# Performance work log

Hardware: AMD Instinct MI355X
Metric: run time of the kernel (lower is better)

Reference implementation:

```python
import jax, jax.numpy as jnp
import numpy as np

RRELU_SLOPE = (1.0 / 8.0 + 1.0 / 3.0) / 2.0  # F.rrelu eval mode
N_ENT, N_REL2, H, E, B, T = 20000, 460, 128, 400000, 1024, 8


def _lin(x, W, b):
    return x @ W.T + b  # torch nn.Linear convention


def _gru_cell(x, h, w_ih, w_hh, b_ih, b_hh):
    gi = x @ w_ih.T + b_ih
    gh = h @ w_hh.T + b_hh
    i_r, i_z, i_n = jnp.split(gi, 3, axis=1)
    h_r, h_z, h_n = jnp.split(gh, 3, axis=1)
    r = jax.nn.sigmoid(i_r + h_r)
    z = jax.nn.sigmoid(i_z + h_z)
    n = jnp.tanh(i_n + r * h_n)
    return (1.0 - z) * n + z * h


def setup_inputs() -> dict:
    key = jax.random.key(0)
    ks = jax.random.split(key, 24)
    s = 0.02
    inp = {
        'ent_emb': jax.random.normal(ks[0], (N_ENT, H), jnp.float32),
        'rel_emb': jax.random.normal(ks[1], (N_REL2, H), jnp.float32),
        'weight_neighbor': jax.random.normal(ks[2], (H, H), jnp.float32) * s,
        'loop_weight': jax.random.normal(ks[3], (H, H), jnp.float32) * s,
        'evolve_loop_weight': jax.random.normal(ks[4], (H, H), jnp.float32) * s,
        'w_ih': jax.random.normal(ks[5], (3 * H, H), jnp.float32) * s,
        'w_hh': jax.random.normal(ks[6], (3 * H, H), jnp.float32) * s,
        'b_ih': jnp.zeros((3 * H,), jnp.float32),
        'b_hh': jnp.zeros((3 * H,), jnp.float32),
        'W_map1': jax.random.normal(ks[7], (2 * H, H), jnp.float32) * s,
        'b_map1': jnp.zeros((2 * H,), jnp.float32),
        'W_map2': jax.random.normal(ks[8], (H, 2 * H), jnp.float32) * s,
        'b_map2': jnp.zeros((H,), jnp.float32),
        'W_h1': jax.random.normal(ks[9], (H, H), jnp.float32) * s,
        'b_h1': jnp.zeros((H,), jnp.float32),
        'W_h2': jax.random.normal(ks[10], (H, H), jnp.float32) * s,
        'b_h2': jnp.zeros((H,), jnp.float32),
        'W_align': jax.random.normal(ks[11], (H, H), jnp.float32) * s,
        'b_align': jnp.zeros((H,), jnp.float32),
        'W_attn': jax.random.normal(ks[12], (H, H), jnp.float32) * s,
        'b_attn': jnp.zeros((H,), jnp.float32),
    }
    u = jax.random.uniform(ks[13], (B, T * N_REL2), jnp.float32)
    mask = jax.random.uniform(ks[14], (B, T * N_REL2)) > 0.7  # sparse history
    inp['partial_embeding'] = u * mask
    inp['edge_src'] = jax.random.randint(ks[15], (E,), 0, N_ENT, jnp.int32)
    inp['edge_dst'] = jax.random.randint(ks[16], (E,), 0, N_ENT, jnp.int32)
    inp['edge_type'] = jax.random.randint(ks[17], (E,), 0, N_REL2, jnp.int32)
    sub = jax.random.randint(ks[18], (B,), 0, N_ENT, jnp.int32)
    rel = jax.random.randint(ks[19], (B,), 0, N_REL2, jnp.int32)
    obj = jax.random.randint(ks[20], (B,), 0, N_ENT, jnp.int32)
    inp['triples'] = jnp.stack([sub, rel, obj], axis=1)
    return inp


def reference(ent_emb, rel_emb, weight_neighbor, loop_weight, evolve_loop_weight,
              w_ih, w_hh, b_ih, b_hh, W_map1, b_map1, W_map2, b_map2,
              W_h1, b_h1, W_h2, b_h2, W_align, b_align, W_attn, b_attn,
              partial_embeding, edge_src, edge_dst, edge_type, triples):
    # ---- UnionRGCNLayer: gather-transform-scatter ----
    h = ent_emb
    msg = (h[edge_src] + rel_emb[edge_type]) @ weight_neighbor          # [E, H]
    agg = jax.ops.segment_sum(msg, edge_dst, num_segments=N_ENT)        # [N, H]
    deg = jax.ops.segment_sum(jnp.ones((edge_dst.shape[0],), h.dtype), edge_dst,
                              num_segments=N_ENT)
    norm = jnp.where(deg > 0, 1.0 / jnp.where(deg > 0, deg, 1.0), 0.0)[:, None]
    loop = jnp.where((deg > 0)[:, None], h @ loop_weight, h @ evolve_loop_weight)
    x = agg * norm + loop
    pre_emb = jnp.where(x >= 0, x, x * RRELU_SLOPE)                     # rrelu (eval)

    # ---- PathPredictor.forward_back ----
    mapped_rel = _lin(_lin(rel_emb, W_map1, b_map1), W_map2, b_map2)    # [2R, H]
    q_rel = mapped_rel[triples[:, 1]]                                   # [B, H]
    A = _lin(q_rel, W_attn, b_attn) @ mapped_rel.T                      # [B, 2R]
    hist = partial_embeding.reshape(B, T, N_REL2).transpose(1, 0, 2)    # [T, B, 2R]

    def step(gh, cur):
        attn = cur * A
        attn = jax.nn.softmax(jnp.where(attn == 0, -1e9, attn), axis=1)
        rel_path = attn @ mapped_rel                                    # [B, H]
        return _gru_cell(rel_path, gh, w_ih, w_hh, b_ih, b_hh), None

    gru_hidden, _ = jax.lax.scan(step, jnp.zeros((B, H), pre_emb.dtype), hist)
    predicted_hist = 0.1 * _lin(_lin(q_rel, W_h1, b_h1), W_h2, b_h2) + q_rel
    match_loss = jnp.mean((predicted_hist - gru_hidden) ** 2)

    # ---- forward_forth, distmult scoring ----
    gh2 = _gru_cell(q_rel, predicted_hist, w_ih, w_hh, b_ih, b_hh)      # [B, H]
    sub_emb = pre_emb[triples[:, 0]]
    aligned_all = _lin(pre_emb, W_align, b_align)                       # [N, H]
    score_ = (_lin(sub_emb, W_align, b_align) * gh2) @ aligned_all.T    # [B, N]
    score = jax.nn.sigmoid(score_)
    # BCE(score, one_hot(obj)) without materializing labels:
    logp = jax.nn.log_sigmoid(score_)
    log1mp = jax.nn.log_sigmoid(-score_)
    total = -jnp.sum(log1mp)
    rows = jnp.arange(B)
    total = total + jnp.sum(log1mp[rows, triples[:, 2]] - logp[rows, triples[:, 2]])
    path_loss = total / (B * N_ENT)
    return score, match_loss, path_loss
```

## Files before the change

kernel.cpp:

```cpp
#include <hip/hip_runtime.h>

typedef unsigned short u16;
typedef unsigned int u32;
typedef __attribute__((ext_vector_type(8))) short bf8v;
typedef __attribute__((ext_vector_type(4))) float f4v;

#define RRELU_SLOPE 0.22916666667f

__device__ inline float bf2f(u16 u){ unsigned int i = ((unsigned int)u) << 16; float f; __builtin_memcpy(&f, &i, 4); return f; }
__device__ inline u16 f2bf(float f){ unsigned int i; __builtin_memcpy(&i, &f, 4); unsigned int r = (i + 0x7fffu + ((i >> 16) & 1u)) >> 16; return (u16)r; }
__device__ inline float fsigm(float x){ return 1.f / (1.f + __expf(-x)); }
__device__ inline float ftanh(float x){ return 2.f / (1.f + __expf(-2.f * x)) - 1.f; }

__global__ __launch_bounds__(256) void prep_k(
    const float* __restrict__ Wn, const float* __restrict__ Wl, const float* __restrict__ We,
    const float* __restrict__ wih, const float* __restrict__ whh,
    const float* __restrict__ m1, const float* __restrict__ m2,
    const float* __restrict__ h1, const float* __restrict__ h2,
    const float* __restrict__ attn, const float* __restrict__ alg, const float* __restrict__ rel,
    u16* __restrict__ Bcat, u16* __restrict__ wihb, u16* __restrict__ whhb,
    u16* __restrict__ m1b, u16* __restrict__ m2b, u16* __restrict__ h1b, u16* __restrict__ h2b,
    u16* __restrict__ attnb, u16* __restrict__ algb, u16* __restrict__ relb)
{
    int id = blockIdx.x * 256 + threadIdx.x;
    if (id < 49152) {
        int n = id / 384, k = id % 384;
        float v = (k < 128) ? Wn[k*128 + n] : (k < 256 ? Wl[(k-128)*128 + n] : We[(k-256)*128 + n]);
        Bcat[id] = f2bf(v); return;
    }
    id -= 49152;
    if (id < 49152) { wihb[id] = f2bf(wih[id]); return; } id -= 49152;
    if (id < 49152) { whhb[id] = f2bf(whh[id]); return; } id -= 49152;
    if (id < 32768) { m1b[id]  = f2bf(m1[id]);  return; } id -= 32768;
    if (id < 32768) { m2b[id]  = f2bf(m2[id]);  return; } id -= 32768;
    if (id < 16384) { h1b[id]  = f2bf(h1[id]);  return; } id -= 16384;
    if (id < 16384) { h2b[id]  = f2bf(h2[id]);  return; } id -= 16384;
    if (id < 16384) { attnb[id]= f2bf(attn[id]);return; } id -= 16384;
    if (id < 16384) { algb[id] = f2bf(alg[id]); return; } id -= 16384;
    if (id < 58880) { relb[id] = f2bf(rel[id]); return; }
}

__global__ __launch_bounds__(256) void entcast_k(
    const float* __restrict__ ent, u16* __restrict__ entb)
{
    int id = blockIdx.x * 256 + threadIdx.x;
    entb[id] = f2bf(ent[id]);
}

__global__ __launch_bounds__(256) void hist_k(
    const int* __restrict__ dst, int* __restrict__ hist, int E)
{
    int e = blockIdx.x * 256 + threadIdx.x;
    if (e < E) atomicAdd(&hist[dst[e]], 1);
}

__global__ __launch_bounds__(1024) void scan_k(
    const int* __restrict__ hist, int* __restrict__ starts, int* __restrict__ cursor)
{
    __shared__ int part[1024];
    int t = threadIdx.x;
    int base = t * 20;
    int s = 0;
    for (int j = 0; j < 20; ++j) { int idx = base + j; if (idx < 20000) s += hist[idx]; }
    part[t] = s;
    __syncthreads();
    for (int off = 1; off < 1024; off <<= 1) {
        int v = (t >= off) ? part[t - off] : 0;
        __syncthreads();
        part[t] += v;
        __syncthreads();
    }
    int run = (t > 0) ? part[t - 1] : 0;
    for (int j = 0; j < 20; ++j) {
        int idx = base + j;
        if (idx < 20000) { starts[idx] = run; cursor[idx] = run; run += hist[idx]; }
    }
    if (t == 1023) starts[20000] = run;
}

__global__ __launch_bounds__(256) void scatter_k(
    const int* __restrict__ src, const int* __restrict__ dst, const int* __restrict__ typ,
    int* __restrict__ cursor, int2* __restrict__ spack, int E)
{
    int e = blockIdx.x * 256 + threadIdx.x;
    if (e >= E) return;
    int d = dst[e];
    int p = atomicAdd(&cursor[d], 1);
    spack[p] = make_int2(src[e], typ[e]);
}

__global__ __launch_bounds__(64) void agg_acat_k(
    const int2* __restrict__ spack, const int* __restrict__ starts,
    const u32* __restrict__ hb, const u32* __restrict__ rb, u32* __restrict__ Acat32)
{
    int i = blockIdx.x;
    int lane = threadIdx.x;
    int s0 = starts[i], s1 = starts[i + 1];
    float sx = 0.f, sy = 0.f;
    for (int e = s0; e < s1; ++e) {
        int2 st = spack[e];
        u32 a = hb[(long)st.x * 64 + lane];
        u32 r = rb[(long)st.y * 64 + lane];
        sx += bf2f((u16)(a & 0xffff)) + bf2f((u16)(r & 0xffff));
        sy += bf2f((u16)(a >> 16))    + bf2f((u16)(r >> 16));
    }
    bool has = s1 > s0;
    float nrm = has ? 1.f / (float)(s1 - s0) : 0.f;
    u32 hv = hb[(long)i * 64 + lane];
    u32 agg = (u32)f2bf(sx * nrm) | ((u32)f2bf(sy * nrm) << 16);
    long o = (long)i * 192 + lane;
    Acat32[o]       = agg;
    Acat32[o + 64]  = has ? hv : 0u;
    Acat32[o + 128] = has ? 0u : hv;
}

__global__ __launch_bounds__(256) void gemm_nt(
    const u16* __restrict__ A, const u16* __restrict__ B, const float* __restrict__ bias,
    float* __restrict__ Cf, u16* __restrict__ Cbf, u16* __restrict__ CT,
    const u16* __restrict__ residb, const int* __restrict__ arows,
    int M, int N, int K, int lda, int ldb, int ldc, int ldct, int arow_stride,
    float rscale, int epi)
{
    int tid = threadIdx.x;
    int wave = tid >> 6, lane = tid & 63;
    int ln = lane & 15, q = lane >> 4;
    int bm = blockIdx.y * 64 + wave * 16;
    int bn = blockIdx.x * 64;
    int am = bm + ln; if (am >= M) am = M - 1;
    long ar = arows ? (long)arows[(long)am * arow_stride] : (long)am;
    const u16* Ap = A + ar * lda;
    int br[4];
#pragma unroll
    for (int nt = 0; nt < 4; ++nt) { int n = bn + nt*16 + ln; br[nt] = (n < N) ? n : (N - 1); }
    f4v acc[4] = {};
    for (int kc = 0; kc < K; kc += 32) {
        bf8v af = *(const bf8v*)(Ap + kc + q*8);
#pragma unroll
        for (int nt = 0; nt < 4; ++nt) {
            bf8v bv = *(const bf8v*)(B + (long)br[nt]*ldb + kc + q*8);
            acc[nt] = __builtin_amdgcn_mfma_f32_16x16x32_bf16(af, bv, acc[nt], 0, 0, 0);
        }
    }
#pragma unroll
    for (int nt = 0; nt < 4; ++nt) {
        int n = bn + nt*16 + ln;
        if (n >= N) continue;
        float bv = bias ? bias[n] : 0.f;
#pragma unroll
        for (int r = 0; r < 4; ++r) {
            int m = bm + q*4 + r;
            if (m >= M) continue;
            float v = acc[nt][r] + bv;
            if (epi == 1) v = (v >= 0.f) ? v : v * RRELU_SLOPE;
            if (residb)  v = rscale * v + bf2f(residb[(long)m*ldc + n]);
            long ci = (long)m*ldc + n;
            if (Cf)  Cf[ci]  = v;
            if (Cbf) Cbf[ci] = f2bf(v);
            if (CT)  CT[(long)n*ldct + m] = f2bf(v);
        }
    }
}

__global__ __launch_bounds__(256) void qrel_k(
    const u16* __restrict__ mapb, const int* __restrict__ trip,
    u16* __restrict__ qrelb, u16* __restrict__ X)
{
    int id = blockIdx.x * 256 + threadIdx.x;
    int b = id >> 7, k = id & 127;
    int r = trip[b*3 + 1];
    u16 v = mapb[r*128 + k];
    qrelb[id] = v;
    X[(long)(8192 + b)*128 + k] = v;
}

__global__ __launch_bounds__(64) void softmax_k(
    const float* __restrict__ Amat, const float* __restrict__ part, u16* __restrict__ Xattn)
{
    int row = blockIdx.x;
    int t = row >> 10, b = row & 1023;
    int lane = threadIdx.x;
    const float* arow = Amat + (long)b*460;
    const float* crow = part + (long)b*3680 + t*460;
    float v[8], e[8];
    float m = -1e30f;
#pragma unroll
    for (int i = 0; i < 8; ++i) {
        int r = i*64 + lane;
        e[i] = 0.f;
        if (r < 460) {
            float x = crow[r] * arow[r];
            x = (x == 0.f) ? -1e9f : x;
            v[i] = x; m = fmaxf(m, x);
        } else v[i] = -1e30f;
    }
#pragma unroll
    for (int off = 32; off; off >>= 1) m = fmaxf(m, __shfl_xor(m, off));
    float sum = 0.f;
#pragma unroll
    for (int i = 0; i < 8; ++i) {
        int r = i*64 + lane;
        if (r < 460) { e[i] = __expf(v[i] - m); sum += e[i]; }
    }
#pragma unroll
    for (int off = 32; off; off >>= 1) sum += __shfl_xor(sum, off);
    float inv = 1.f / sum;
#pragma unroll
    for (int i = 0; i < 8; ++i) {
        int r = i*64 + lane;
        if (r < 460)      Xattn[(long)row*480 + r] = f2bf(e[i] * inv);
        else if (r < 480) Xattn[(long)row*480 + r] = 0;
    }
}

__global__ __launch_bounds__(256) void gru_k(
    const float* __restrict__ gi, const u16* __restrict__ whhb, const float* __restrict__ bhh,
    const float* __restrict__ pred, float* __restrict__ gh2, float* __restrict__ match_acc)
{
    __shared__ u16  hbf[16][136];
    __shared__ float hf [4][128];
    __shared__ float ghl[4][388];
    __shared__ float red[4];
    int tid = threadIdx.x;
    int wave = tid >> 6, lane = tid & 63;
    int ln = lane & 15, q = lane >> 4;
    int bb = blockIdx.x * 4;
    for (int i = tid; i < 16*136; i += 256) hbf[i/136][i%136] = 0;
    for (int i = tid; i < 4*128; i += 256) hf[i>>7][i&127] = 0.f;
    bf8v bfrag[6][4];
#pragma unroll
    for (int nt = 0; nt < 6; ++nt)
#pragma unroll
        for (int kc = 0; kc < 4; ++kc)
            bfrag[nt][kc] = *(const bf8v*)(whhb + (long)(wave*96 + nt*16 + ln)*128 + kc*32 + q*8);
    int k = tid & 127;
    float br = bhh[k], bz = bhh[128 + k], bn_ = bhh[256 + k];
    __syncthreads();
    float msum = 0.f;
    for (int t = 0; t <= 8; ++t) {
        float gr[2], gz[2], gn[2], pv[2];
        long girow0 = (t < 8) ? ((long)t*1024 + bb) : (8192 + bb);
#pragma unroll
        for (int it = 0; it < 2; ++it) {
            int m = it*2 + (tid >> 7);
            const float* gp = gi + (girow0 + m)*384;
            gr[it] = gp[k]; gz[it] = gp[128 + k]; gn[it] = gp[256 + k];
            pv[it] = (t >= 7) ? pred[(long)(bb + m)*128 + k] : 0.f;
        }
        if (t == 8) {
#pragma unroll
            for (int it = 0; it < 2; ++it) {
                int m = it*2 + (tid >> 7);
                hf[m][k] = pv[it]; hbf[m][k] = f2bf(pv[it]);
            }
            __syncthreads();
        }
        f4v acc[6] = {};
#pragma unroll
        for (int kc = 0; kc < 4; ++kc) {
            bf8v af = *(const bf8v*)&hbf[ln][kc*32 + q*8];
#pragma unroll
            for (int nt = 0; nt < 6; ++nt)
                acc[nt] = __builtin_amdgcn_mfma_f32_16x16x32_bf16(af, bfrag[nt][kc], acc[nt], 0, 0, 0);
        }
        if (q == 0) {
#pragma unroll
            for (int nt = 0; nt < 6; ++nt)
#pragma unroll
                for (int r = 0; r < 4; ++r)
                    ghl[r][wave*96 + nt*16 + ln] = acc[nt][r];
        }
        __syncthreads();
#pragma unroll
        for (int it = 0; it < 2; ++it) {
            int m = it*2 + (tid >> 7);
            float rr = fsigm(gr[it] + ghl[m][k] + br);
            float zz = fsigm(gz[it] + ghl[m][128 + k] + bz);
            float nn = ftanh(gn[it] + rr * (ghl[m][256 + k] + bn_));
            float hn = (1.f - zz) * nn + zz * hf[m][k];
            if (t == 7) { float d = pv[it] - hn; msum += d*d; }
            if (t == 8) { gh2[(long)(bb + m)*128 + k] = hn; }
            else        { hf[m][k] = hn; hbf[m][k] = f2bf(hn); }
        }
        __syncthreads();
    }
#pragma unroll
    for (int off = 32; off; off >>= 1) msum += __shfl_down(msum, off);
    if (lane == 0) red[wave] = msum;
    __syncthreads();
    if (tid == 0) atomicAdd(match_acc, red[0] + red[1] + red[2] + red[3]);
}

__global__ __launch_bounds__(256) void vmul_k(
    const float* __restrict__ subl, const float* __restrict__ gh2, u16* __restrict__ V)
{
    int id = blockIdx.x * 256 + threadIdx.x;
    V[id] = f2bf(subl[id] * gh2[id]);
}

__global__ __launch_bounds__(256) void score_k(
    const u16* __restrict__ V, const u16* __restrict__ AL,
    float* __restrict__ out, float* __restrict__ sp_acc, int N)
{
    int tid = threadIdx.x;
    int wave = tid >> 6, lane = tid & 63;
    int ln = lane & 15, q = lane >> 4;
    int bm = blockIdx.y * 128 + (wave >> 1) * 64;
    int bn = blockIdx.x * 128 + (wave & 1) * 64;
    int br[4];
#pragma unroll
    for (int nt = 0; nt < 4; ++nt) { int n = bn + nt*16 + ln; br[nt] = (n < N) ? n : (N - 1); }
    f4v acc[4][4] = {};
    for (int kc = 0; kc < 128; kc += 32) {
        bf8v a[4], b[4];
#pragma unroll
        for (int mt = 0; mt < 4; ++mt)
            a[mt] = *(const bf8v*)(V + (long)(bm + mt*16 + ln)*128 + kc + q*8);
#pragma unroll
        for (int nt = 0; nt < 4; ++nt)
            b[nt] = *(const bf8v*)(AL + (long)br[nt]*128 + kc + q*8);
#pragma unroll
        for (int mt = 0; mt < 4; ++mt)
#pragma unroll
            for (int nt = 0; nt < 4; ++nt)
                acc[mt][nt] = __builtin_amdgcn_mfma_f32_16x16x32_bf16(a[mt], b[nt], acc[mt][nt], 0, 0, 0);
    }
    float lsum = 0.f;
#pragma unroll
    for (int mt = 0; mt < 4; ++mt)
#pragma unroll
    for (int nt = 0; nt < 4; ++nt) {
        int n = bn + nt*16 + ln;
        if (n >= N) continue;
#pragma unroll
        for (int r = 0; r < 4; ++r) {
            int m = bm + mt*16 + q*4 + r;
            float s = acc[mt][nt][r];
            float e = __expf(-fabsf(s));
            float inv = 1.f / (1.f + e);
            __builtin_nontemporal_store((s >= 0.f) ? inv : e * inv, &out[(long)m*N + n]);
            lsum += fmaxf(s, 0.f) + __logf(1.f + e);
        }
    }
#pragma unroll
    for (int off = 32; off; off >>= 1) lsum += __shfl_xor(lsum, off);
    __shared__ float red[4];
    if (lane == 0) red[wave] = lsum;
    __syncthreads();
    if (tid == 0) atomicAdd(sp_acc, red[0] + red[1] + red[2] + red[3]);
}

__global__ __launch_bounds__(64) void objdot_k(
    const u16* __restrict__ V, const u16* __restrict__ AL, const int* __restrict__ trip,
    float* __restrict__ obj_acc)
{
    int b = blockIdx.x, lane = threadIdx.x;
    int obj = trip[b*3 + 2];
    const u16* v = V + (long)b*128;
    const u16* a = AL + (long)obj*128;
    float s = 0.f;
    for (int k = lane; k < 128; k += 64) s += bf2f(v[k]) * bf2f(a[k]);
    for (int off = 32; off; off >>= 1) s += __shfl_down(s, off);
    if (lane == 0) atomicAdd(obj_acc, -s);
}

__global__ void final_k(const float* __restrict__ acc, float* __restrict__ out)
{
    out[20480000] = acc[0] / (1024.f * 128.f);
    out[20480001] = (acc[1] + acc[2]) / (1024.f * 20000.f);
}

extern "C" void kernel_launch(void* const* d_in, const int* in_sizes, int n_in,
                              void* d_out, int out_size, void* d_ws, size_t ws_size,
                              hipStream_t stream)
{
    const float* ent  = (const float*)d_in[0];
    const float* rel  = (const float*)d_in[1];
    const float* Wn   = (const float*)d_in[2];
    const float* Wl   = (const float*)d_in[3];
    const float* We   = (const float*)d_in[4];
    const float* wih  = (const float*)d_in[5];
    const float* whh  = (const float*)d_in[6];
    const float* b_ih = (const float*)d_in[7];
    const float* b_hh = (const float*)d_in[8];
    const float* Wm1  = (const float*)d_in[9];
    const float* bm1  = (const float*)d_in[10];
    const float* Wm2  = (const float*)d_in[11];
    const float* bm2  = (const float*)d_in[12];
    const float* Wh1  = (const float*)d_in[13];
    const float* bh1  = (const float*)d_in[14];
    const float* Wh2  = (const float*)d_in[15];
    const float* bh2  = (const float*)d_in[16];
    const float* Wal  = (const float*)d_in[17];
    const float* bal  = (const float*)d_in[18];
    const float* Wat  = (const float*)d_in[19];
    const float* bat  = (const float*)d_in[20];
    const float* part = (const float*)d_in[21];
    const int* esrc   = (const int*)d_in[22];
    const int* edst   = (const int*)d_in[23];
    const int* etyp   = (const int*)d_in[24];
    const int* trip   = (const int*)d_in[25];
    float* out = (float*)d_out;
    const int E = in_sizes[22];

    char* ws = (char*)d_ws;
    size_t off = 0;
    auto alloc = [&](size_t bytes) { size_t o = off; off = (off + bytes + 255) & ~(size_t)255; return o; };

    size_t o_acc   = alloc(256);
    size_t o_hist  = alloc(20000 * 4);
    size_t o_mapT  = alloc(128 * 480 * 2);
    size_t zend = off;
    size_t o_starts= alloc(20004 * 4);
    size_t o_cur   = alloc(20000 * 4);
    size_t o_spack = alloc((size_t)E * 8);
    size_t o_entb  = alloc((size_t)20000 * 128 * 2);
    size_t o_acat  = alloc((size_t)20000 * 384 * 2);
    size_t o_pre   = alloc((size_t)20000 * 128 * 2);
    size_t o_aln   = alloc((size_t)20000 * 128 * 2);
    size_t o_bcat  = alloc(128 * 384 * 2);
    size_t o_wih   = alloc(384 * 128 * 2);
    size_t o_whh   = alloc(384 * 128 * 2);
    size_t o_m1    = alloc(256 * 128 * 2);
    size_t o_m2    = alloc(128 * 256 * 2);
    size_t o_h1    = alloc(128 * 128 * 2);
    size_t o_h2    = alloc(128 * 128 * 2);
    size_t o_at    = alloc(128 * 128 * 2);
    size_t o_al    = alloc(128 * 128 * 2);
    size_t o_rel   = alloc(460 * 128 * 2);
    size_t o_t1    = alloc(460 * 256 * 2);
    size_t o_map   = alloc(460 * 128 * 2);
    size_t o_qrel  = alloc(1024 * 128 * 2);
    size_t o_atq   = alloc(1024 * 128 * 2);
    size_t o_th1   = alloc(1024 * 128 * 2);
    size_t o_pred  = alloc(1024 * 128 * 4);
    size_t o_amat  = alloc((size_t)1024 * 460 * 4);
    size_t o_xat   = alloc((size_t)8192 * 480 * 2);
    size_t o_X     = alloc((size_t)9216 * 128 * 2);
    size_t o_gi    = alloc((size_t)9216 * 384 * 4);
    size_t o_subl  = alloc(1024 * 128 * 4);
    size_t o_gh2   = alloc(1024 * 128 * 4);
    size_t o_V     = alloc(1024 * 128 * 2);

    float* accp  = (float*)(ws + o_acc);
    int* histp   = (int*)(ws + o_hist);
    u16* mapT    = (u16*)(ws + o_mapT);
    int* startsp = (int*)(ws + o_starts);
    int* curp    = (int*)(ws + o_cur);
    int2* spack  = (int2*)(ws + o_spack);
    u16* entb    = (u16*)(ws + o_entb);
    u16* acat    = (u16*)(ws + o_acat);
    u16* preb    = (u16*)(ws + o_pre);
    u16* alnb    = (u16*)(ws + o_aln);
    u16* bcat    = (u16*)(ws + o_bcat);
    u16* wihb    = (u16*)(ws + o_wih);
    u16* whhb    = (u16*)(ws + o_whh);
    u16* m1b     = (u16*)(ws + o_m1);
    u16* m2b     = (u16*)(ws + o_m2);
    u16* h1b     = (u16*)(ws + o_h1);
    u16* h2b     = (u16*)(ws + o_h2);
    u16* atb     = (u16*)(ws + o_at);
    u16* alb     = (u16*)(ws + o_al);
    u16* relb    = (u16*)(ws + o_rel);
    u16* t1b     = (u16*)(ws + o_t1);
    u16* mapb    = (u16*)(ws + o_map);
    u16* qrelb   = (u16*)(ws + o_qrel);
    u16* atqb    = (u16*)(ws + o_atq);
    u16* th1b    = (u16*)(ws + o_th1);
    float* predf = (float*)(ws + o_pred);
    float* amat  = (float*)(ws + o_amat);
    u16* xat     = (u16*)(ws + o_xat);
    u16* Xb      = (u16*)(ws + o_X);
    float* gif   = (float*)(ws + o_gi);
    float* subl  = (float*)(ws + o_subl);
    float* gh2f  = (float*)(ws + o_gh2);
    u16* Vb      = (u16*)(ws + o_V);

    hipMemsetAsync(ws, 0, zend, stream);

    prep_k<<<1318, 256, 0, stream>>>(Wn, Wl, We, wih, whh, Wm1, Wm2, Wh1, Wh2, Wat, Wal, rel,
                                     bcat, wihb, whhb, m1b, m2b, h1b, h2b, atb, alb, relb);
    entcast_k<<<10000, 256, 0, stream>>>(ent, entb);

    int eb = (E + 255) / 256;
    hist_k<<<eb, 256, 0, stream>>>(edst, histp, E);
    scan_k<<<1, 1024, 0, stream>>>(histp, startsp, curp);
    scatter_k<<<eb, 256, 0, stream>>>(esrc, edst, etyp, curp, spack, E);
    agg_acat_k<<<20000, 64, 0, stream>>>(spack, startsp, (const u32*)entb, (const u32*)relb, (u32*)acat);

    gemm_nt<<<dim3(2, 313), 256, 0, stream>>>(acat, bcat, nullptr, nullptr, preb, nullptr, nullptr, nullptr,
                                              20000, 128, 384, 384, 384, 128, 0, 0, 0.f, 1);
    gemm_nt<<<dim3(2, 313), 256, 0, stream>>>(preb, alb, bal, nullptr, alnb, nullptr, nullptr, nullptr,
                                              20000, 128, 128, 128, 128, 128, 0, 0, 0.f, 0);
    gemm_nt<<<dim3(4, 8), 256, 0, stream>>>(relb, m1b, bm1, nullptr, t1b, nullptr, nullptr, nullptr,
                                            460, 256, 128, 128, 128, 256, 0, 0, 0.f, 0);
    gemm_nt<<<dim3(2, 8), 256, 0, stream>>>(t1b, m2b, bm2, nullptr, mapb, mapT, nullptr, nullptr,
                                            460, 128, 256, 256, 256, 128, 480, 0, 0.f, 0);

    qrel_k<<<512, 256, 0, stream>>>(mapb, trip, qrelb, Xb);

    gemm_nt<<<dim3(2, 16), 256, 0, stream>>>(qrelb, atb, bat, nullptr, atqb, nullptr, nullptr, nullptr,
                                             1024, 128, 128, 128, 128, 128, 0, 0, 0.f, 0);
    gemm_nt<<<dim3(2, 16), 256, 0, stream>>>(qrelb, h1b, bh1, nullptr, th1b, nullptr, nullptr, nullptr,
                                             1024, 128, 128, 128, 128, 128, 0, 0, 0.f, 0);
    gemm_nt<<<dim3(2, 16), 256, 0, stream>>>(th1b, h2b, bh2, predf, nullptr, nullptr, qrelb, nullptr,
                                             1024, 128, 128, 128, 128, 128, 0, 0, 0.1f, 0);
    gemm_nt<<<dim3(8, 16), 256, 0, stream>>>(atqb, mapb, nullptr, amat, nullptr, nullptr, nullptr, nullptr,
                                             1024, 460, 128, 128, 128, 460, 0, 0, 0.f, 0);

    softmax_k<<<8192, 64, 0, stream>>>(amat, part, xat);

    gemm_nt<<<dim3(2, 128), 256, 0, stream>>>(xat, mapT, nullptr, nullptr, Xb, nullptr, nullptr, nullptr,
                                              8192, 128, 480, 480, 480, 128, 0, 0, 0.f, 0);
    gemm_nt<<<dim3(6, 144), 256, 0, stream>>>(Xb, wihb, b_ih, gif, nullptr, nullptr, nullptr, nullptr,
                                              9216, 384, 128, 128, 128, 384, 0, 0, 0.f, 0);
    gemm_nt<<<dim3(2, 16), 256, 0, stream>>>(preb, alb, bal, subl, nullptr, nullptr, nullptr, trip,
                                             1024, 128, 128, 128, 128, 128, 0, 3, 0.f, 0);

    gru_k<<<256, 256, 0, stream>>>(gif, whhb, b_hh, predf, gh2f, accp + 0);

    vmul_k<<<512, 256, 0, stream>>>(subl, gh2f, Vb);

    score_k<<<dim3(157, 8), 256, 0, stream>>>(Vb, alnb, out, accp + 1, 20000);

    objdot_k<<<1024, 64, 0, stream>>>(Vb, alnb, trip, accp + 2);

    final_k<<<1, 1, 0, stream>>>(accp, out);

    (void)in_sizes; (void)n_in; (void)out_size; (void)ws_size;
}
```

Before: 476.3 us.

## Stage score B tile in LDS and write outputs as coalesced float4 rows

```diff
diff --git a/kernel.cpp b/kernel.cpp
--- a/kernel.cpp
+++ b/kernel.cpp
@@ -297,49 +297,68 @@
     V[id] = f2bf(subl[id] * gh2[id]);
 }
 
-__global__ __launch_bounds__(256) void score_k(
+__global__ __launch_bounds__(256, 4) void score_k(
     const u16* __restrict__ V, const u16* __restrict__ AL,
     float* __restrict__ out, float* __restrict__ sp_acc, int N)
 {
+    __shared__ char smem[35072];
+    u16* Blds = (u16*)smem;
     int tid = threadIdx.x;
     int wave = tid >> 6, lane = tid & 63;
     int ln = lane & 15, q = lane >> 4;
-    int bm = blockIdx.y * 128 + (wave >> 1) * 64;
-    int bn = blockIdx.x * 128 + (wave & 1) * 64;
-    int br[4];
-#pragma unroll
-    for (int nt = 0; nt < 4; ++nt) { int n = bn + nt*16 + ln; br[nt] = (n < N) ? n : (N - 1); }
-    f4v acc[4][4] = {};
-    for (int kc = 0; kc < 128; kc += 32) {
-        bf8v a[4], b[4];
-#pragma unroll
-        for (int mt = 0; mt < 4; ++mt)
-            a[mt] = *(const bf8v*)(V + (long)(bm + mt*16 + ln)*128 + kc + q*8);
+    int bm = blockIdx.y * 128 + wave * 32;
+    int bn = blockIdx.x * 64;
+#pragma unroll
+    for (int j = 0; j < 4; ++j) {
+        int idx = j*256 + tid;
+        int row = idx >> 4, off = (idx & 15) * 8;
+        int gr = bn + row; if (gr >= N) gr = N - 1;
+        bf8v v = *(const bf8v*)(AL + (long)gr*128 + off);
+        *(bf8v*)(Blds + row*136 + off) = v;
+    }
+    __syncthreads();
+    f4v acc[2][4] = {};
+#pragma unroll
+    for (int kc = 0; kc < 4; ++kc) {
+        bf8v a[2], b[4];
+#pragma unroll
+        for (int mt = 0; mt < 2; ++mt)
+            a[mt] = *(const bf8v*)(V + (long)(bm + mt*16 + ln)*128 + kc*32 + q*8);
 #pragma unroll
         for (int nt = 0; nt < 4; ++nt)
-            b[nt] = *(const bf8v*)(AL + (long)br[nt]*128 + kc + q*8);
-#pragma unroll
-        for (int mt = 0; mt < 4; ++mt)
+            b[nt] = *(const bf8v*)(Blds + (nt*16 + ln)*136 + kc*32 + q*8);
+#pragma unroll
+        for (int mt = 0; mt < 2; ++mt)
 #pragma unroll
             for (int nt = 0; nt < 4; ++nt)
                 acc[mt][nt] = __builtin_amdgcn_mfma_f32_16x16x32_bf16(a[mt], b[nt], acc[mt][nt], 0, 0, 0);
     }
+    __syncthreads();
+    float* Ep = (float*)smem + wave * (32*68);
     float lsum = 0.f;
 #pragma unroll
-    for (int mt = 0; mt < 4; ++mt)
+    for (int mt = 0; mt < 2; ++mt)
 #pragma unroll
     for (int nt = 0; nt < 4; ++nt) {
         int n = bn + nt*16 + ln;
-        if (n >= N) continue;
+        bool ok = n < N;
 #pragma unroll
         for (int r = 0; r < 4; ++r) {
-            int m = bm + mt*16 + q*4 + r;
             float s = acc[mt][nt][r];
             float e = __expf(-fabsf(s));
             float inv = 1.f / (1.f + e);
-            __builtin_nontemporal_store((s >= 0.f) ? inv : e * inv, &out[(long)m*N + n]);
-            lsum += fmaxf(s, 0.f) + __logf(1.f + e);
-        }
+            Ep[(mt*16 + q*4 + r)*68 + nt*16 + ln] = (s >= 0.f) ? inv : e * inv;
+            if (ok) lsum += fmaxf(s, 0.f) + __logf(1.f + e);
+        }
+    }
+    __syncthreads();
+#pragma unroll
+    for (int p = 0; p < 8; ++p) {
+        int row = p*4 + (lane >> 4);
+        int c4 = (lane & 15) * 4;
+        f4v v = *(const f4v*)(Ep + row*68 + c4);
+        int n = bn + c4;
+        if (n < N) *(f4v*)(&out[(long)(bm + row)*N + n]) = v;
     }
 #pragma unroll
     for (int off = 32; off; off >>= 1) lsum += __shfl_xor(lsum, off);
@@ -520,7 +539,7 @@
 
     vmul_k<<<512, 256, 0, stream>>>(subl, gh2f, Vb);
 
-    score_k<<<dim3(157, 8), 256, 0, stream>>>(Vb, alnb, out, accp + 1, 20000);
+    score_k<<<dim3(313, 8), 256, 0, stream>>>(Vb, alnb, out, accp + 1, 20000);
 
     objdot_k<<<1024, 64, 0, stream>>>(Vb, alnb, trip, accp + 2);
 
```

Measured after the change: 482.8 us. No clear change (+1.4%).
